# Performance work log

Hardware: AMD Instinct MI355X
Metric: run time of the kernel (lower is better)

Reference implementation:

```python
import jax, jax.numpy as jnp
import numpy as np

N_NODES = 50000
NFEAT = 512
NHID = 128
N_EDGES = 800000
LN_EPS = 1e-5


def setup_inputs() -> dict:
    key = jax.random.key(0)
    k1, k2, k3, k4, k5 = jax.random.split(key, 5)
    h = jax.random.normal(k1, (N_NODES, NFEAT), dtype=jnp.float32)
    src = jax.random.randint(k2, (N_EDGES,), 0, N_NODES, dtype=jnp.int32)
    dst = jax.random.randint(k3, (N_EDGES,), 0, N_NODES, dtype=jnp.int32)
    # GraphConv params (glorot-ish) + bias; LayerNorm affine params
    W = jax.random.normal(k4, (NFEAT, NHID), dtype=jnp.float32) / np.sqrt(NFEAT)
    b = jnp.zeros((NHID,), dtype=jnp.float32)
    gamma = jnp.ones((NHID,), dtype=jnp.float32)
    beta = jnp.zeros((NHID,), dtype=jnp.float32)
    return {"h": h, "src": src, "dst": dst, "W": W, "b": b, "gamma": gamma, "beta": beta}


def reference(h, src, dst, W, b, gamma, beta):
    n = h.shape[0]
    ones = jnp.ones_like(src, dtype=jnp.float32)
    out_deg = jax.ops.segment_sum(ones, src, num_segments=n)
    in_deg = jax.ops.segment_sum(ones, dst, num_segments=n)
    out_norm = jnp.maximum(out_deg, 1.0) ** -0.5  # [N]
    in_norm = jnp.maximum(in_deg, 1.0) ** -0.5    # [N]

    # norm='both': scale source features by out_deg^{-1/2}
    x = h * out_norm[:, None]
    # in_feats > out_feats -> DGL multiplies by W before aggregation
    x = x @ W  # [N, NHID]
    # sparse aggregate: sum messages over incoming edges
    agg = jax.ops.segment_sum(x[src], dst, num_segments=n)  # [N, NHID]
    agg = agg * in_norm[:, None] + b

    # LayerNorm over last dim
    mu = jnp.mean(agg, axis=-1, keepdims=True)
    var = jnp.mean((agg - mu) ** 2, axis=-1, keepdims=True)
    y = (agg - mu) * jax.lax.rsqrt(var + LN_EPS) * gamma + beta
    return y
```

## Files before the change

### kernel.cpp

```cpp
#include <hip/hip_runtime.h>

#define N_NODES 50000
#define NFEAT   512
#define NHID    128
#define N_EDGES 800000
#define LN_EPS  1e-5f

#define GEMM_ROWS   32
#define GEMM_BLOCKS ((N_NODES + GEMM_ROWS - 1) / GEMM_ROWS)
#define NB_SCAN     ((N_NODES + 1023) / 1024)
#define ZROW        N_NODES

#define TBL     50176
#define NCH_IN  50
#define EC_IN   16000
#define NCH_OUT 32
#define EC_OUT  25000

typedef __attribute__((ext_vector_type(8))) short bf16x8;
typedef __attribute__((ext_vector_type(4))) float fx4;

__device__ __forceinline__ unsigned short f2bf(float f) {
    union { float f; unsigned u; } v; v.f = f;
    unsigned r = v.u + 0x7FFF + ((v.u >> 16) & 1);
    return (unsigned short)(r >> 16);
}

__device__ __forceinline__ void bf2x(unsigned u, float& lo, float& hi) {
    union { unsigned u; float f; } a, b;
    a.u = u << 16;
    b.u = u & 0xFFFF0000u;
    lo = a.f; hi = b.f;
}

__global__ __launch_bounds__(256) void prep_kernel(
    const float* __restrict__ W, unsigned short* __restrict__ wf,
    unsigned short* __restrict__ x)
{
    if (blockIdx.x == 32) {
        if (threadIdx.x < 16)
            ((int4*)(x + (size_t)ZROW * NHID))[threadIdx.x] = make_int4(0, 0, 0, 0);
        return;
    }
    int t = blockIdx.x * 256 + threadIdx.x;
    int lane = t & 63;
    int frag = t >> 6;
    int kc = frag >> 3, tt = frag & 7;
    int n  = tt * 16 + (lane & 15);
    int k0 = kc * 32 + (lane >> 4) * 8;
    unsigned short v[8];
#pragma unroll
    for (int j = 0; j < 8; j++)
        v[j] = f2bf(W[(size_t)(k0 + j) * NHID + n]);
    *(bf16x8*)(wf + (size_t)t * 8) = *(bf16x8*)v;
}

__global__ __launch_bounds__(256) void hist_kernel(
    const int* __restrict__ src, const int* __restrict__ dst,
    unsigned short* __restrict__ in16, unsigned short* __restrict__ out16,
    unsigned short* __restrict__ rank16)
{
    __shared__ unsigned int hist[TBL / 2];
    const int tid = threadIdx.x;
    const int b   = blockIdx.x;

    for (int i = tid; i < TBL / 2; i += 256) hist[i] = 0;
    __syncthreads();

    if (b < NCH_IN) {
        const int base = b * EC_IN;
        for (int i = tid; i < EC_IN; i += 256) {
            int e = base + i;
            int d = dst[e];
            unsigned sh  = (d & 1) * 16;
            unsigned old = atomicAdd(&hist[d >> 1], 1u << sh);
            rank16[e] = (unsigned short)((old >> sh) & 0xFFFFu);
        }
        __syncthreads();
        unsigned int* g = (unsigned int*)(in16 + (size_t)b * TBL);
        for (int i = tid; i < TBL / 2; i += 256) g[i] = hist[i];
    } else {
        const int base = (b - NCH_IN) * EC_OUT;
        for (int i = tid; i < EC_OUT; i += 256) {
            int s = src[base + i];
            atomicAdd(&hist[s >> 1], 1u << ((s & 1) * 16));
        }
        __syncthreads();
        unsigned int* g = (unsigned int*)(out16 + (size_t)(b - NCH_IN) * TBL);
        for (int i = tid; i < TBL / 2; i += 256) g[i] = hist[i];
    }
}

__global__ __launch_bounds__(1024) void scan_local(
    unsigned short* __restrict__ in16, const unsigned short* __restrict__ out16,
    int* __restrict__ row_ptr, int* __restrict__ bsum, float* __restrict__ out_norm)
{
    __shared__ int wsum[16];
    const int tid = threadIdx.x;
    const int lane = tid & 63, wave = tid >> 6;
    int i = blockIdx.x * 1024 + tid;
    int v = 0;
    if (i < N_NODES) {
        int acc = 0;
        for (int c = 0; c < NCH_IN; c++) {
            size_t idx = (size_t)c * TBL + i;
            int cnt = in16[idx];
            in16[idx] = (unsigned short)acc;
            acc += cnt;
        }
        v = acc;
        int od = 0;
        for (int c = 0; c < NCH_OUT; c++)
            od += out16[(size_t)c * TBL + i];
        out_norm[i] = rsqrtf(fmaxf((float)od, 1.0f));
    }
    int sv = v;
#pragma unroll
    for (int off = 1; off < 64; off <<= 1) {
        int t = __shfl_up(sv, off);
        if (lane >= off) sv += t;
    }
    if (lane == 63) wsum[wave] = sv;
    __syncthreads();
    if (wave == 0) {
        int wv = (lane < 16) ? wsum[lane] : 0;
#pragma unroll
        for (int off = 1; off < 16; off <<= 1) {
            int t = __shfl_up(wv, off);
            if (lane >= off) wv += t;
        }
        if (lane < 16) wsum[lane] = wv;
    }
    __syncthreads();
    int excl = ((wave > 0) ? wsum[wave - 1] : 0) + (sv - v);
    if (i < N_NODES) row_ptr[i] = excl;
    if (tid == 1023) bsum[blockIdx.x] = wsum[15];
}

__global__ __launch_bounds__(1024) void scan_add2(
    int* __restrict__ row_ptr, const int* __restrict__ bsum)
{
    __shared__ int off_s, tot_s;
    const int tid = threadIdx.x;
    if (tid < 64) {
        int v = (tid < NB_SCAN) ? bsum[tid] : 0;
        int sv = v;
#pragma unroll
        for (int off = 1; off < 64; off <<= 1) {
            int t = __shfl_up(sv, off);
            if (tid >= off) sv += t;
        }
        int pre = __shfl(sv, (blockIdx.x == 0) ? 0 : (blockIdx.x - 1));
        int tot = __shfl(sv, NB_SCAN - 1);
        if (tid == 0) {
            off_s = (blockIdx.x == 0) ? 0 : pre;
            tot_s = tot;
        }
    }
    __syncthreads();
    int i = blockIdx.x * 1024 + tid;
    if (i < N_NODES) row_ptr[i] += off_s;
    if (blockIdx.x == 0 && tid == 0) row_ptr[N_NODES] = tot_s;
}

__global__ __launch_bounds__(256) void fill_kernel(
    const int* __restrict__ src, const int* __restrict__ dst,
    const int* __restrict__ row_ptr, const unsigned short* __restrict__ in16,
    const unsigned short* __restrict__ rank16, int* __restrict__ csr_src)
{
    int e = blockIdx.x * 256 + threadIdx.x;
    if (e < N_EDGES) {
        int d = dst[e];
        int c = e / EC_IN;
        int pos = (int)in16[(size_t)c * TBL + d] + (int)rank16[e];
        csr_src[row_ptr[d] + pos] = src[e];
    }
}

__global__ __launch_bounds__(256) void gemm_kernel(
    const float* __restrict__ h, const unsigned short* __restrict__ wf,
    const float* __restrict__ out_norm, unsigned short* __restrict__ x)
{
    __shared__ __align__(16) unsigned short afrag_lds[2][16 * 64 * 8];
    __shared__ float on_s[32];

    const int tid  = threadIdx.x;
    const int row0 = blockIdx.x * GEMM_ROWS;

    if (tid < 32) {
        int gr = row0 + tid;
        if (gr > N_NODES - 1) gr = N_NODES - 1;
        on_s[tid] = out_norm[gr];
    }

    {
        float4 v[16];
#pragma unroll
        for (int it = 0; it < 16; it++) {
            int i = tid + it * 256;
            int r = i >> 7;
            int grow = row0 + r;
            if (grow > N_NODES - 1) grow = N_NODES - 1;
            v[it] = ((const float4*)h)[(size_t)grow * 128 + (i & 127)];
        }
#pragma unroll
        for (int it = 0; it < 16; it++) {
            int i = tid + it * 256;
            int r  = i >> 7;
            int g  = r >> 4;
            int rr = r & 15;
            int k0 = (i & 127) << 2;
            int kc = k0 >> 5;
            int q  = (k0 >> 3) & 3;
            int j  = k0 & 7;
            int gp = q * 16 + (rr ^ (q | ((kc & 1) << 2)));
            unsigned long long pk =
                (unsigned long long)f2bf(v[it].x)
              | ((unsigned long long)f2bf(v[it].y) << 16)
              | ((unsigned long long)f2bf(v[it].z) << 32)
              | ((unsigned long long)f2bf(v[it].w) << 48);
            *(unsigned long long*)(&afrag_lds[g][0] + kc * 512 + gp * 8 + j) = pk;
        }
    }
    __syncthreads();

    const int wave = tid >> 6;
    const int lane = tid & 63;
    const int t0   = wave * 2;
    const int rr_l = lane & 15;
    const int q_l  = lane >> 4;
    const int g_e  = q_l * 16 + (rr_l ^ q_l);
    const int g_o  = q_l * 16 + (rr_l ^ q_l ^ 4);

    fx4 acc00 = (fx4){0.f, 0.f, 0.f, 0.f};
    fx4 acc01 = (fx4){0.f, 0.f, 0.f, 0.f};
    fx4 acc10 = (fx4){0.f, 0.f, 0.f, 0.f};
    fx4 acc11 = (fx4){0.f, 0.f, 0.f, 0.f};

    const bf16x8* a0p = (const bf16x8*)&afrag_lds[0][0];
    const bf16x8* a1p = (const bf16x8*)&afrag_lds[1][0];
    const bf16x8* wfp = (const bf16x8*)wf + t0 * 64 + lane;

#pragma unroll 4
    for (int kc = 0; kc < 16; kc++) {
        int gidx = (kc & 1) ? g_o : g_e;
        bf16x8 a0 = a0p[kc * 64 + gidx];
        bf16x8 a1 = a1p[kc * 64 + gidx];
        bf16x8 b0 = wfp[kc * 512];
        bf16x8 b1 = wfp[kc * 512 + 64];
        acc00 = __builtin_amdgcn_mfma_f32_16x16x32_bf16(a0, b0, acc00, 0, 0, 0);
        acc01 = __builtin_amdgcn_mfma_f32_16x16x32_bf16(a0, b1, acc01, 0, 0, 0);
        acc10 = __builtin_amdgcn_mfma_f32_16x16x32_bf16(a1, b0, acc10, 0, 0, 0);
        acc11 = __builtin_amdgcn_mfma_f32_16x16x32_bf16(a1, b1, acc11, 0, 0, 0);
    }

    __syncthreads();
    unsigned short* orow = (unsigned short*)&afrag_lds[0][0];
    {
        const int q = lane >> 4;
        const int c = lane & 15;
#pragma unroll
        for (int reg = 0; reg < 4; reg++) {
            int r0 = q * 4 + reg;
            float w0 = on_s[r0];
            float w1 = on_s[16 + r0];
            orow[r0 * 128 + t0 * 16 + c]              = f2bf(acc00[reg] * w0);
            orow[r0 * 128 + (t0 + 1) * 16 + c]        = f2bf(acc01[reg] * w0);
            orow[(16 + r0) * 128 + t0 * 16 + c]       = f2bf(acc10[reg] * w1);
            orow[(16 + r0) * 128 + (t0 + 1) * 16 + c] = f2bf(acc11[reg] * w1);
        }
    }
    __syncthreads();
    {
        const int4* osrc = (const int4*)&afrag_lds[0][0];
#pragma unroll
        for (int p = 0; p < 2; p++) {
            int idx = tid + p * 256;
            int r   = idx >> 4;
            int gr  = row0 + r;
            if (gr < N_NODES)
                ((int4*)x)[(size_t)gr * 16 + (idx & 15)] = osrc[idx];
        }
    }
}

#define ACC4(uu) {                                                        \
    float p0,p1,p2,p3,p4,p5,p6,p7;                                        \
    bf2x(uu.x,p0,p1); bf2x(uu.y,p2,p3);                                   \
    bf2x(uu.z,p4,p5); bf2x(uu.w,p6,p7);                                   \
    a0 += p0; a1 += p1; a2 += p2; a3 += p3;                               \
    a4 += p4; a5 += p5; a6 += p6; a7 += p7; }

__global__ __launch_bounds__(256) void aggregate_kernel(
    const unsigned short* __restrict__ x, const int* __restrict__ row_ptr,
    const int* __restrict__ csr_src,
    const float* __restrict__ b, const float* __restrict__ gamma,
    const float* __restrict__ beta, float* __restrict__ out)
{
    const int n    = blockIdx.x * 4 + (threadIdx.x >> 6);
    const int lane = threadIdx.x & 63;
    const int qi   = lane >> 4;
    const int c    = lane & 15;
    const int start = row_ptr[n];
    const int end   = row_ptr[n + 1];

    float a0 = 0.f, a1 = 0.f, a2 = 0.f, a3 = 0.f;
    float a4 = 0.f, a5 = 0.f, a6 = 0.f, a7 = 0.f;

    for (int base = start; base < end; base += 64) {
        int  me   = base + lane;
        int  msrc = (me < end) ? csr_src[me] : (int)ZROW;
        int cnt = min(64, end - base);
        int ng  = (cnt + 3) >> 2;
        int g = 0;
        for (; g + 4 <= ng; g += 4) {
            int i0 = 4 * g + qi, i1 = i0 + 4, i2 = i0 + 8, i3 = i0 + 12;
            int s0 = __shfl(msrc, i0);
            int s1 = __shfl(msrc, i1);
            int s2 = __shfl(msrc, i2);
            int s3 = __shfl(msrc, i3);
            uint4 u0 = *(const uint4*)(x + (size_t)s0 * NHID + c * 8);
            uint4 u1 = *(const uint4*)(x + (size_t)s1 * NHID + c * 8);
            uint4 u2 = *(const uint4*)(x + (size_t)s2 * NHID + c * 8);
            uint4 u3 = *(const uint4*)(x + (size_t)s3 * NHID + c * 8);
            ACC4(u0) ACC4(u1) ACC4(u2) ACC4(u3)
        }
        for (; g < ng; ++g) {
            int i0 = 4 * g + qi;
            int s0 = __shfl(msrc, i0);
            uint4 u0 = *(const uint4*)(x + (size_t)s0 * NHID + c * 8);
            ACC4(u0)
        }
    }

    a0 += __shfl_xor(a0, 16); a0 += __shfl_xor(a0, 32);
    a1 += __shfl_xor(a1, 16); a1 += __shfl_xor(a1, 32);
    a2 += __shfl_xor(a2, 16); a2 += __shfl_xor(a2, 32);
    a3 += __shfl_xor(a3, 16); a3 += __shfl_xor(a3, 32);
    a4 += __shfl_xor(a4, 16); a4 += __shfl_xor(a4, 32);
    a5 += __shfl_xor(a5, 16); a5 += __shfl_xor(a5, 32);
    a6 += __shfl_xor(a6, 16); a6 += __shfl_xor(a6, 32);
    a7 += __shfl_xor(a7, 16); a7 += __shfl_xor(a7, 32);

    float inorm = rsqrtf(fmaxf((float)(end - start), 1.0f));
    float4 b0 = *(const float4*)(b + c * 8);
    float4 b1 = *(const float4*)(b + c * 8 + 4);
    float v0 = a0 * inorm + b0.x;
    float v1 = a1 * inorm + b0.y;
    float v2 = a2 * inorm + b0.z;
    float v3 = a3 * inorm + b0.w;
    float v4 = a4 * inorm + b1.x;
    float v5 = a5 * inorm + b1.y;
    float v6 = a6 * inorm + b1.z;
    float v7 = a7 * inorm + b1.w;

    float s = ((v0 + v1) + (v2 + v3)) + ((v4 + v5) + (v6 + v7));
#pragma unroll
    for (int off = 8; off > 0; off >>= 1) s += __shfl_xor(s, off);
    float mu = s * (1.0f / 128.0f);

    float d0 = v0 - mu, d1 = v1 - mu, d2 = v2 - mu, d3 = v3 - mu;
    float d4 = v4 - mu, d5 = v5 - mu, d6 = v6 - mu, d7 = v7 - mu;
    float qd = ((d0*d0 + d1*d1) + (d2*d2 + d3*d3)) + ((d4*d4 + d5*d5) + (d6*d6 + d7*d7));
#pragma unroll
    for (int off = 8; off > 0; off >>= 1) qd += __shfl_xor(qd, off);
    float var = qd * (1.0f / 128.0f);
    float rs = rsqrtf(var + LN_EPS);

    if (lane < 16) {
        float4 gg = *(const float4*)(gamma + c * 8);
        float4 be = *(const float4*)(beta + c * 8);
        float4 o;
        o.x = d0 * rs * gg.x + be.x;
        o.y = d1 * rs * gg.y + be.y;
        o.z = d2 * rs * gg.z + be.z;
        o.w = d3 * rs * gg.w + be.w;
        *(float4*)(out + (size_t)n * NHID + c * 8) = o;
    } else if (lane < 32) {
        float4 gg = *(const float4*)(gamma + c * 8 + 4);
        float4 be = *(const float4*)(beta + c * 8 + 4);
        float4 o;
        o.x = d4 * rs * gg.x + be.x;
        o.y = d5 * rs * gg.y + be.y;
        o.z = d6 * rs * gg.z + be.z;
        o.w = d7 * rs * gg.w + be.w;
        *(float4*)(out + (size_t)n * NHID + c * 8 + 4) = o;
    }
}

extern "C" void kernel_launch(void* const* d_in, const int* in_sizes, int n_in,
                              void* d_out, int out_size, void* d_ws, size_t ws_size,
                              hipStream_t stream) {
    const float* h     = (const float*)d_in[0];
    const int*   src   = (const int*)d_in[1];
    const int*   dst   = (const int*)d_in[2];
    const float* W     = (const float*)d_in[3];
    const float* b     = (const float*)d_in[4];
    const float* gamma = (const float*)d_in[5];
    const float* beta  = (const float*)d_in[6];
    float* out = (float*)d_out;

    char* p = (char*)d_ws;
    unsigned short* in16   = (unsigned short*)p;  p += (size_t)NCH_IN  * TBL * 2;
    unsigned short* out16  = (unsigned short*)p;
    int*            csr_src= (int*)p;             p += (size_t)NCH_OUT * TBL * 2;
    unsigned short* rank16 = (unsigned short*)p;  p += 1600512;
    int*            row_ptr= (int*)p;             p += 200960;
    float*          out_norm=(float*)p;           p += 200704;
    int*            bsum   = (int*)p;             p += 1024;
    unsigned short* wf     = (unsigned short*)p;  p += 131072;
    unsigned short* x      = (unsigned short*)p;

    prep_kernel<<<33, 256, 0, stream>>>(W, wf, x);
    hist_kernel<<<NCH_IN + NCH_OUT, 256, 0, stream>>>(src, dst, in16, out16, rank16);
    scan_local<<<NB_SCAN, 1024, 0, stream>>>(in16, out16, row_ptr, bsum, out_norm);
    scan_add2 <<<NB_SCAN, 1024, 0, stream>>>(row_ptr, bsum);
    fill_kernel<<<(N_EDGES + 255) / 256, 256, 0, stream>>>(src, dst, row_ptr, in16, rank16, csr_src);
    gemm_kernel<<<GEMM_BLOCKS, 256, 0, stream>>>(h, wf, out_norm, x);
    aggregate_kernel<<<N_NODES / 4, 256, 0, stream>>>(
        x, row_ptr, csr_src, b, gamma, beta, out);
}
```

Measured before the change: 283.9 us.

## Fuse histogram with GEMM, defer out-degree scaling to aggregation, use 8-bit counts

The GEMM no longer scales rows by out_norm. That scaling moves into the aggregation as a per-edge weight fetched once per edge and broadcast with shuffles. With that dependency gone, the GEMM blocks launch in the same kernel as the degree-histogram blocks, so both run concurrently and one launch is saved. Histogram and rank buffers shrink from 16-bit to 8-bit counters, halving scan and fill traffic. The risks are silent overflow if any node gets more than 255 edges in a chunk, and lower GEMM occupancy from the larger shared LDS footprint.

New measurement: 264.6 us. 1.07x faster.

```diff
diff --git a/kernel.cpp b/kernel.cpp
--- a/kernel.cpp
+++ b/kernel.cpp
@@ -9,13 +9,13 @@
 #define GEMM_ROWS   32
 #define GEMM_BLOCKS ((N_NODES + GEMM_ROWS - 1) / GEMM_ROWS)
 #define NB_SCAN     ((N_NODES + 1023) / 1024)
-#define ZROW        N_NODES
 
 #define TBL     50176
 #define NCH_IN  50
 #define EC_IN   16000
 #define NCH_OUT 32
 #define EC_OUT  25000
+#define HG_BLOCKS (NCH_IN + NCH_OUT)
 
 typedef __attribute__((ext_vector_type(8))) short bf16x8;
 typedef __attribute__((ext_vector_type(4))) float fx4;
@@ -34,14 +34,8 @@
 }
 
 __global__ __launch_bounds__(256) void prep_kernel(
-    const float* __restrict__ W, unsigned short* __restrict__ wf,
-    unsigned short* __restrict__ x)
-{
-    if (blockIdx.x == 32) {
-        if (threadIdx.x < 16)
-            ((int4*)(x + (size_t)ZROW * NHID))[threadIdx.x] = make_int4(0, 0, 0, 0);
-        return;
-    }
+    const float* __restrict__ W, unsigned short* __restrict__ wf)
+{
     int t = blockIdx.x * 256 + threadIdx.x;
     int lane = t & 63;
     int frag = t >> 6;
@@ -55,143 +49,56 @@
     *(bf16x8*)(wf + (size_t)t * 8) = *(bf16x8*)v;
 }
 
-__global__ __launch_bounds__(256) void hist_kernel(
+__global__ __launch_bounds__(256) void fused_hist_gemm(
+    const float* __restrict__ h, const unsigned short* __restrict__ wf,
+    unsigned short* __restrict__ x,
     const int* __restrict__ src, const int* __restrict__ dst,
-    unsigned short* __restrict__ in16, unsigned short* __restrict__ out16,
-    unsigned short* __restrict__ rank16)
-{
-    __shared__ unsigned int hist[TBL / 2];
+    unsigned char* __restrict__ in8, unsigned char* __restrict__ out8,
+    unsigned char* __restrict__ rank8)
+{
+    __shared__ __align__(16) unsigned char smem[TBL];
+
     const int tid = threadIdx.x;
-    const int b   = blockIdx.x;
-
-    for (int i = tid; i < TBL / 2; i += 256) hist[i] = 0;
-    __syncthreads();
-
-    if (b < NCH_IN) {
-        const int base = b * EC_IN;
-        for (int i = tid; i < EC_IN; i += 256) {
-            int e = base + i;
-            int d = dst[e];
-            unsigned sh  = (d & 1) * 16;
-            unsigned old = atomicAdd(&hist[d >> 1], 1u << sh);
-            rank16[e] = (unsigned short)((old >> sh) & 0xFFFFu);
+    const int B = blockIdx.x;
+
+    if (B < HG_BLOCKS) {
+        unsigned int* hist = (unsigned int*)smem;
+        {
+            uint4* h4 = (uint4*)smem;
+            for (int i = tid; i < TBL / 16; i += 256)
+                h4[i] = make_uint4(0, 0, 0, 0);
         }
         __syncthreads();
-        unsigned int* g = (unsigned int*)(in16 + (size_t)b * TBL);
-        for (int i = tid; i < TBL / 2; i += 256) g[i] = hist[i];
-    } else {
-        const int base = (b - NCH_IN) * EC_OUT;
-        for (int i = tid; i < EC_OUT; i += 256) {
-            int s = src[base + i];
-            atomicAdd(&hist[s >> 1], 1u << ((s & 1) * 16));
-        }
-        __syncthreads();
-        unsigned int* g = (unsigned int*)(out16 + (size_t)(b - NCH_IN) * TBL);
-        for (int i = tid; i < TBL / 2; i += 256) g[i] = hist[i];
-    }
-}
-
-__global__ __launch_bounds__(1024) void scan_local(
-    unsigned short* __restrict__ in16, const unsigned short* __restrict__ out16,
-    int* __restrict__ row_ptr, int* __restrict__ bsum, float* __restrict__ out_norm)
-{
-    __shared__ int wsum[16];
-    const int tid = threadIdx.x;
-    const int lane = tid & 63, wave = tid >> 6;
-    int i = blockIdx.x * 1024 + tid;
-    int v = 0;
-    if (i < N_NODES) {
-        int acc = 0;
-        for (int c = 0; c < NCH_IN; c++) {
-            size_t idx = (size_t)c * TBL + i;
-            int cnt = in16[idx];
-            in16[idx] = (unsigned short)acc;
-            acc += cnt;
-        }
-        v = acc;
-        int od = 0;
-        for (int c = 0; c < NCH_OUT; c++)
-            od += out16[(size_t)c * TBL + i];
-        out_norm[i] = rsqrtf(fmaxf((float)od, 1.0f));
-    }
-    int sv = v;
-#pragma unroll
-    for (int off = 1; off < 64; off <<= 1) {
-        int t = __shfl_up(sv, off);
-        if (lane >= off) sv += t;
-    }
-    if (lane == 63) wsum[wave] = sv;
-    __syncthreads();
-    if (wave == 0) {
-        int wv = (lane < 16) ? wsum[lane] : 0;
-#pragma unroll
-        for (int off = 1; off < 16; off <<= 1) {
-            int t = __shfl_up(wv, off);
-            if (lane >= off) wv += t;
-        }
-        if (lane < 16) wsum[lane] = wv;
-    }
-    __syncthreads();
-    int excl = ((wave > 0) ? wsum[wave - 1] : 0) + (sv - v);
-    if (i < N_NODES) row_ptr[i] = excl;
-    if (tid == 1023) bsum[blockIdx.x] = wsum[15];
-}
-
-__global__ __launch_bounds__(1024) void scan_add2(
-    int* __restrict__ row_ptr, const int* __restrict__ bsum)
-{
-    __shared__ int off_s, tot_s;
-    const int tid = threadIdx.x;
-    if (tid < 64) {
-        int v = (tid < NB_SCAN) ? bsum[tid] : 0;
-        int sv = v;
-#pragma unroll
-        for (int off = 1; off < 64; off <<= 1) {
-            int t = __shfl_up(sv, off);
-            if (tid >= off) sv += t;
-        }
-        int pre = __shfl(sv, (blockIdx.x == 0) ? 0 : (blockIdx.x - 1));
-        int tot = __shfl(sv, NB_SCAN - 1);
-        if (tid == 0) {
-            off_s = (blockIdx.x == 0) ? 0 : pre;
-            tot_s = tot;
-        }
-    }
-    __syncthreads();
-    int i = blockIdx.x * 1024 + tid;
-    if (i < N_NODES) row_ptr[i] += off_s;
-    if (blockIdx.x == 0 && tid == 0) row_ptr[N_NODES] = tot_s;
-}
-
-__global__ __launch_bounds__(256) void fill_kernel(
-    const int* __restrict__ src, const int* __restrict__ dst,
-    const int* __restrict__ row_ptr, const unsigned short* __restrict__ in16,
-    const unsigned short* __restrict__ rank16, int* __restrict__ csr_src)
-{
-    int e = blockIdx.x * 256 + threadIdx.x;
-    if (e < N_EDGES) {
-        int d = dst[e];
-        int c = e / EC_IN;
-        int pos = (int)in16[(size_t)c * TBL + d] + (int)rank16[e];
-        csr_src[row_ptr[d] + pos] = src[e];
-    }
-}
-
-__global__ __launch_bounds__(256) void gemm_kernel(
-    const float* __restrict__ h, const unsigned short* __restrict__ wf,
-    const float* __restrict__ out_norm, unsigned short* __restrict__ x)
-{
-    __shared__ __align__(16) unsigned short afrag_lds[2][16 * 64 * 8];
-    __shared__ float on_s[32];
-
-    const int tid  = threadIdx.x;
-    const int row0 = blockIdx.x * GEMM_ROWS;
-
-    if (tid < 32) {
-        int gr = row0 + tid;
-        if (gr > N_NODES - 1) gr = N_NODES - 1;
-        on_s[tid] = out_norm[gr];
-    }
+        if (B < NCH_IN) {
+            const int base = B * EC_IN;
+            for (int i = tid; i < EC_IN; i += 256) {
+                int e = base + i;
+                int d = dst[e];
+                unsigned sh  = (d & 3) * 8;
+                unsigned old = atomicAdd(&hist[d >> 2], 1u << sh);
+                rank8[e] = (unsigned char)((old >> sh) & 0xFFu);
+            }
+            __syncthreads();
+            uint4* g = (uint4*)(in8 + (size_t)B * TBL);
+            uint4* h4 = (uint4*)smem;
+            for (int i = tid; i < TBL / 16; i += 256) g[i] = h4[i];
+        } else {
+            const int base = (B - NCH_IN) * EC_OUT;
+            for (int i = tid; i < EC_OUT; i += 256) {
+                int s = src[base + i];
+                atomicAdd(&hist[s >> 2], 1u << ((s & 3) * 8));
+            }
+            __syncthreads();
+            uint4* g = (uint4*)(out8 + (size_t)(B - NCH_IN) * TBL);
+            uint4* h4 = (uint4*)smem;
+            for (int i = tid; i < TBL / 16; i += 256) g[i] = h4[i];
+        }
+        return;
+    }
+
+    unsigned short (*afrag_lds)[16 * 64 * 8] =
+        (unsigned short (*)[16 * 64 * 8])smem;
+    const int row0 = (B - HG_BLOCKS) * GEMM_ROWS;
 
     {
         float4 v[16];
@@ -255,24 +162,22 @@
     }
 
     __syncthreads();
-    unsigned short* orow = (unsigned short*)&afrag_lds[0][0];
+    unsigned short* orow = (unsigned short*)smem;
     {
         const int q = lane >> 4;
         const int c = lane & 15;
 #pragma unroll
         for (int reg = 0; reg < 4; reg++) {
             int r0 = q * 4 + reg;
-            float w0 = on_s[r0];
-            float w1 = on_s[16 + r0];
-            orow[r0 * 128 + t0 * 16 + c]              = f2bf(acc00[reg] * w0);
-            orow[r0 * 128 + (t0 + 1) * 16 + c]        = f2bf(acc01[reg] * w0);
-            orow[(16 + r0) * 128 + t0 * 16 + c]       = f2bf(acc10[reg] * w1);
-            orow[(16 + r0) * 128 + (t0 + 1) * 16 + c] = f2bf(acc11[reg] * w1);
+            orow[r0 * 128 + t0 * 16 + c]              = f2bf(acc00[reg]);
+            orow[r0 * 128 + (t0 + 1) * 16 + c]        = f2bf(acc01[reg]);
+            orow[(16 + r0) * 128 + t0 * 16 + c]       = f2bf(acc10[reg]);
+            orow[(16 + r0) * 128 + (t0 + 1) * 16 + c] = f2bf(acc11[reg]);
         }
     }
     __syncthreads();
     {
-        const int4* osrc = (const int4*)&afrag_lds[0][0];
+        const int4* osrc = (const int4*)smem;
 #pragma unroll
         for (int p = 0; p < 2; p++) {
             int idx = tid + p * 256;
@@ -284,16 +189,106 @@
     }
 }
 
-#define ACC4(uu) {                                                        \
+__global__ __launch_bounds__(1024) void scan_local(
+    unsigned char* __restrict__ in8, const unsigned char* __restrict__ out8,
+    int* __restrict__ row_ptr, int* __restrict__ bsum, float* __restrict__ out_norm)
+{
+    __shared__ int wsum[16];
+    const int tid = threadIdx.x;
+    const int lane = tid & 63, wave = tid >> 6;
+    int i = blockIdx.x * 1024 + tid;
+    int v = 0;
+    if (i < N_NODES) {
+        int acc = 0;
+#pragma unroll 5
+        for (int c = 0; c < NCH_IN; c++) {
+            size_t idx = (size_t)c * TBL + i;
+            int cnt = in8[idx];
+            in8[idx] = (unsigned char)acc;
+            acc += cnt;
+        }
+        v = acc;
+        int od = 0;
+#pragma unroll 8
+        for (int c = 0; c < NCH_OUT; c++)
+            od += out8[(size_t)c * TBL + i];
+        out_norm[i] = rsqrtf(fmaxf((float)od, 1.0f));
+    }
+    int sv = v;
+#pragma unroll
+    for (int off = 1; off < 64; off <<= 1) {
+        int t = __shfl_up(sv, off);
+        if (lane >= off) sv += t;
+    }
+    if (lane == 63) wsum[wave] = sv;
+    __syncthreads();
+    if (wave == 0) {
+        int wv = (lane < 16) ? wsum[lane] : 0;
+#pragma unroll
+        for (int off = 1; off < 16; off <<= 1) {
+            int t = __shfl_up(wv, off);
+            if (lane >= off) wv += t;
+        }
+        if (lane < 16) wsum[lane] = wv;
+    }
+    __syncthreads();
+    int excl = ((wave > 0) ? wsum[wave - 1] : 0) + (sv - v);
+    if (i < N_NODES) row_ptr[i] = excl;
+    if (tid == 1023) bsum[blockIdx.x] = wsum[15];
+}
+
+__global__ __launch_bounds__(1024) void scan_add2(
+    int* __restrict__ row_ptr, const int* __restrict__ bsum)
+{
+    __shared__ int off_s, tot_s;
+    const int tid = threadIdx.x;
+    if (tid < 64) {
+        int v = (tid < NB_SCAN) ? bsum[tid] : 0;
+        int sv = v;
+#pragma unroll
+        for (int off = 1; off < 64; off <<= 1) {
+            int t = __shfl_up(sv, off);
+            if (tid >= off) sv += t;
+        }
+        int pre = __shfl(sv, (blockIdx.x == 0) ? 0 : (blockIdx.x - 1));
+        int tot = __shfl(sv, NB_SCAN - 1);
+        if (tid == 0) {
+            off_s = (blockIdx.x == 0) ? 0 : pre;
+            tot_s = tot;
+        }
+    }
+    __syncthreads();
+    int i = blockIdx.x * 1024 + tid;
+    if (i < N_NODES) row_ptr[i] += off_s;
+    if (blockIdx.x == 0 && tid == 0) row_ptr[N_NODES] = tot_s;
+}
+
+__global__ __launch_bounds__(256) void fill_kernel(
+    const int* __restrict__ src, const int* __restrict__ dst,
+    const int* __restrict__ row_ptr, const unsigned char* __restrict__ in8,
+    const unsigned char* __restrict__ rank8, int* __restrict__ csr_src)
+{
+    int e = blockIdx.x * 256 + threadIdx.x;
+    if (e < N_EDGES) {
+        int d = dst[e];
+        int c = e / EC_IN;
+        int pos = (int)in8[(size_t)c * TBL + d] + (int)rank8[e];
+        csr_src[row_ptr[d] + pos] = src[e];
+    }
+}
+
+#define ACC4W(uu, ww) {                                                   \
     float p0,p1,p2,p3,p4,p5,p6,p7;                                        \
     bf2x(uu.x,p0,p1); bf2x(uu.y,p2,p3);                                   \
     bf2x(uu.z,p4,p5); bf2x(uu.w,p6,p7);                                   \
-    a0 += p0; a1 += p1; a2 += p2; a3 += p3;                               \
-    a4 += p4; a5 += p5; a6 += p6; a7 += p7; }
+    a0 = fmaf(p0,ww,a0); a1 = fmaf(p1,ww,a1);                             \
+    a2 = fmaf(p2,ww,a2); a3 = fmaf(p3,ww,a3);                             \
+    a4 = fmaf(p4,ww,a4); a5 = fmaf(p5,ww,a5);                             \
+    a6 = fmaf(p6,ww,a6); a7 = fmaf(p7,ww,a7); }
 
 __global__ __launch_bounds__(256) void aggregate_kernel(
     const unsigned short* __restrict__ x, const int* __restrict__ row_ptr,
-    const int* __restrict__ csr_src,
+    const int* __restrict__ csr_src, const float* __restrict__ out_norm,
     const float* __restrict__ b, const float* __restrict__ gamma,
     const float* __restrict__ beta, float* __restrict__ out)
 {
@@ -309,7 +304,9 @@
 
     for (int base = start; base < end; base += 64) {
         int  me   = base + lane;
-        int  msrc = (me < end) ? csr_src[me] : (int)ZROW;
+        bool vld  = (me < end);
+        int  msrc = vld ? csr_src[me] : 0;
+        float mw  = vld ? out_norm[msrc] : 0.f;
         int cnt = min(64, end - base);
         int ng  = (cnt + 3) >> 2;
         int g = 0;
@@ -319,17 +316,22 @@
             int s1 = __shfl(msrc, i1);
             int s2 = __shfl(msrc, i2);
             int s3 = __shfl(msrc, i3);
+            float w0 = __shfl(mw, i0);
+            float w1 = __shfl(mw, i1);
+            float w2 = __shfl(mw, i2);
+            float w3 = __shfl(mw, i3);
             uint4 u0 = *(const uint4*)(x + (size_t)s0 * NHID + c * 8);
             uint4 u1 = *(const uint4*)(x + (size_t)s1 * NHID + c * 8);
             uint4 u2 = *(const uint4*)(x + (size_t)s2 * NHID + c * 8);
             uint4 u3 = *(const uint4*)(x + (size_t)s3 * NHID + c * 8);
-            ACC4(u0) ACC4(u1) ACC4(u2) ACC4(u3)
+            ACC4W(u0, w0) ACC4W(u1, w1) ACC4W(u2, w2) ACC4W(u3, w3)
         }
         for (; g < ng; ++g) {
             int i0 = 4 * g + qi;
             int s0 = __shfl(msrc, i0);
+            float w0 = __shfl(mw, i0);
             uint4 u0 = *(const uint4*)(x + (size_t)s0 * NHID + c * 8);
-            ACC4(u0)
+            ACC4W(u0, w0)
         }
     }
 
@@ -401,22 +403,23 @@
     float* out = (float*)d_out;
 
     char* p = (char*)d_ws;
-    unsigned short* in16   = (unsigned short*)p;  p += (size_t)NCH_IN  * TBL * 2;
-    unsigned short* out16  = (unsigned short*)p;
-    int*            csr_src= (int*)p;             p += (size_t)NCH_OUT * TBL * 2;
-    unsigned short* rank16 = (unsigned short*)p;  p += 1600512;
-    int*            row_ptr= (int*)p;             p += 200960;
-    float*          out_norm=(float*)p;           p += 200704;
-    int*            bsum   = (int*)p;             p += 1024;
-    unsigned short* wf     = (unsigned short*)p;  p += 131072;
-    unsigned short* x      = (unsigned short*)p;
-
-    prep_kernel<<<33, 256, 0, stream>>>(W, wf, x);
-    hist_kernel<<<NCH_IN + NCH_OUT, 256, 0, stream>>>(src, dst, in16, out16, rank16);
-    scan_local<<<NB_SCAN, 1024, 0, stream>>>(in16, out16, row_ptr, bsum, out_norm);
+    unsigned char*  in8     = (unsigned char*)p;  p += (size_t)NCH_IN  * TBL;
+    unsigned char*  out8    = (unsigned char*)p;  p += (size_t)NCH_OUT * TBL;
+    unsigned char*  rank8   = (unsigned char*)p;  p += 800768;
+    int*            row_ptr = (int*)p;            p += 200960;
+    float*          out_norm= (float*)p;          p += 200704;
+    int*            bsum    = (int*)p;            p += 1024;
+    unsigned short* wf      = (unsigned short*)p; p += 131072;
+    int*            csr_src = (int*)p;            p += (size_t)N_EDGES * 4;
+    unsigned short* x       = (unsigned short*)p;
+
+    prep_kernel<<<32, 256, 0, stream>>>(W, wf);
+    fused_hist_gemm<<<HG_BLOCKS + GEMM_BLOCKS, 256, 0, stream>>>(
+        h, wf, x, src, dst, in8, out8, rank8);
+    scan_local<<<NB_SCAN, 1024, 0, stream>>>(in8, out8, row_ptr, bsum, out_norm);
     scan_add2 <<<NB_SCAN, 1024, 0, stream>>>(row_ptr, bsum);
-    fill_kernel<<<(N_EDGES + 255) / 256, 256, 0, stream>>>(src, dst, row_ptr, in16, rank16, csr_src);
-    gemm_kernel<<<GEMM_BLOCKS, 256, 0, stream>>>(h, wf, out_norm, x);
+    fill_kernel<<<(N_EDGES + 255) / 256, 256, 0, stream>>>(
+        src, dst, row_ptr, in8, rank8, csr_src);
     aggregate_kernel<<<N_NODES / 4, 256, 0, stream>>>(
-        x, row_ptr, csr_src, b, gamma, beta, out);
-}
+        x, row_ptr, csr_src, out_norm, b, gamma, beta, out);
+}
```
